# Performance work log

Hardware: AMD Instinct MI355X
Metric: run time of the kernel (lower is better)

## Reference

```python
import jax, jax.numpy as jnp
import numpy as np

N, G, C = 32, 197, 768
HEADS = 12
D = C // HEADS          # 64
HH = WW = 14            # spatial grid (L = 196)
F = WW // 2 + 1         # 8 rfft freqs
MLP = 3072
EPS = 1e-6


def _layernorm(x, w, b):
    mu = jnp.mean(x, axis=-1, keepdims=True)
    var = jnp.mean((x - mu) ** 2, axis=-1, keepdims=True)
    return (x - mu) / jnp.sqrt(var + EPS) * w + b


def setup_inputs() -> dict:
    key = jax.random.key(0)
    ks = jax.random.split(key, 16)
    std = 0.02
    return {
        "x": jax.random.normal(ks[0], (N, G, C), dtype=jnp.float32),
        "mixer": std * jax.random.normal(ks[1], (HH, F, C, C, 2), dtype=jnp.float32),
        "Q_w": std * jax.random.normal(ks[2], (D, HEADS, D), dtype=jnp.float32),
        "Q_b": std * jax.random.normal(ks[3], (1, HEADS, 1), dtype=jnp.float32),
        "K_w": std * jax.random.normal(ks[4], (D, HEADS, D), dtype=jnp.float32),
        "K_b": std * jax.random.normal(ks[5], (G, HEADS, 1), dtype=jnp.float32),
        "V_w": std * jax.random.normal(ks[6], (D, HEADS, D), dtype=jnp.float32),
        "V_b": std * jax.random.normal(ks[7], (G, HEADS, 1), dtype=jnp.float32),
        "ln2_w": jnp.ones((C,), dtype=jnp.float32),
        "ln2_b": jnp.zeros((C,), dtype=jnp.float32),
        "w1": std * jax.random.normal(ks[8], (C, MLP), dtype=jnp.float32),
        "b1": jnp.zeros((MLP,), dtype=jnp.float32),
        "w2": std * jax.random.normal(ks[9], (MLP, C), dtype=jnp.float32),
        "b2": jnp.zeros((C,), dtype=jnp.float32),
    }


def reference(x, mixer, Q_w, Q_b, K_w, K_b, V_w, V_b, ln2_w, ln2_b, w1, b1, w2, b2):
    # NOTE: original torch code computes ln_1(input) but discards it (dead code).
    cls = x[:, :1]                       # [N,1,C]
    tok = x[:, 1:]                       # [N,L,C]
    t = tok.reshape(N, HH, WW, C)
    tf = jnp.fft.rfft2(t, axes=(1, 2), norm="ortho")          # [N,H,F,C] complex64
    m = mixer[..., 0] + 1j * mixer[..., 1]                       # [H,F,C,C] complex64
    tf = jnp.einsum("nhfd,hfds->nhfd", tf, m)
    t = jnp.fft.irfft2(tf, s=(HH, WW), axes=(1, 2), norm="ortho").reshape(N, HH * WW, C)
    full = jnp.concatenate([cls, t], axis=1)                     # [N,G,C]
    Q = cls.reshape(N, 1, HEADS, D)
    K = full.reshape(N, G, HEADS, D)
    V = full.reshape(N, G, HEADS, D)
    Q = jnp.einsum("nqhd,xhd->nqhx", Q, Q_w) + Q_b
    K = jnp.einsum("nkhd,xhd->nkhx", K, K_w) + K_b
    V = jnp.einsum("nvhd,xhd->nvhx", V, V_w) + V_b
    A = jnp.einsum("nqhd,nkhd->nhqk", Q, K) / (float(D) ** 0.5)
    A = jax.nn.softmax(A, axis=3)
    new_cls = jnp.einsum("nhqk,nkhd->nqhd", A, V).reshape(N, 1, C)
    xo = jnp.concatenate([new_cls, t], axis=1) + x               # residual (dropout=identity)
    y = _layernorm(xo, ln2_w, ln2_b)
    y = jax.nn.gelu(y @ w1 + b1, approximate=False) @ w2 + b2
    return xo + y
```

## Files before the change

### kernel.cpp

```cpp
#include <hip/hip_runtime.h>
#include <hip/hip_bf16.h>

typedef unsigned short u16;
typedef short bf16x8 __attribute__((ext_vector_type(8)));
typedef float f32x4 __attribute__((ext_vector_type(4)));

#define N_ 32
#define G_ 197
#define C_ 768
#define HEADS_ 12
#define D_ 64
#define HH_ 14
#define FF_ 8
#define MLP_ 3072
#define MPAD 6400
#define MROWS 6304

__device__ __forceinline__ u16 f2bf(float f) {
    unsigned int u = __float_as_uint(f);
    u += 0x7FFF + ((u >> 16) & 1);
    return (u16)(u >> 16);
}

__global__ __launch_bounds__(256) void reduce_mixer(const float* __restrict__ mixer,
                                                    float2* __restrict__ msum) {
    int lane = threadIdx.x & 63;
    size_t widx = (size_t)blockIdx.x * 4 + (threadIdx.x >> 6);
    const float* base = mixer + widx * 1536;
    float re = 0.f, im = 0.f;
#pragma unroll
    for (int it = 0; it < 6; it++) {
        float4 v = *(const float4*)(base + it * 256 + lane * 4);
        re += v.x + v.z;
        im += v.y + v.w;
    }
#pragma unroll
    for (int o = 32; o; o >>= 1) {
        re += __shfl_xor(re, o);
        im += __shfl_xor(im, o);
    }
    if (lane == 0) msum[widx] = make_float2(re, im);
}

__global__ __launch_bounds__(256) void build_k(const float2* __restrict__ msum,
                                               float* __restrict__ kbuf) {
    int d = blockIdx.x;
    int tid = threadIdx.x;
    __shared__ float mre[112], mim[112], ct[14], st[14];
    if (tid < 112) {
        float2 v = msum[(size_t)tid * 768 + d];
        mre[tid] = v.x;
        mim[tid] = v.y;
    }
    if (tid >= 112 && tid < 126) {
        int j = tid - 112;
        float ang = 6.28318530717958647692f * (float)j / 14.f;
        ct[j] = cosf(ang);
        st[j] = sinf(ang);
    }
    __syncthreads();
    if (tid < 196) {
        int da = tid / 14, db = tid % 14;
        float acc = 0.f;
        for (int u = 0; u < 14; u++) {
            int idx = (u * da) % 14;
#pragma unroll
            for (int v = 0; v < 8; v++) {
                float w = (v == 0 || v == 7) ? 1.f : 2.f;
                acc += w * (mre[u * 8 + v] * ct[idx] - mim[u * 8 + v] * st[idx]);
                idx += db;
                if (idx >= 14) idx -= 14;
            }
        }
        kbuf[(size_t)d * 196 + tid] = acc * (1.f / 196.f);
    }
}

__device__ __forceinline__ void conv_proc(int a, int p, int lane, const float* kl,
                                          const float (&tq)[14], float (&ac)[14]) {
    int ra = a - p;
    if (ra < 0) ra += 14;
    const float* kr = &kl[lane * 197 + ra * 14];
    float kq[14];
#pragma unroll
    for (int i = 0; i < 14; i++) kq[i] = kr[i];
#pragma unroll
    for (int b = 0; b < 14; b++)
#pragma unroll
        for (int q = 0; q < 14; q++) ac[b] += tq[q] * kq[(b - q + 14) % 14];
}

__global__ __launch_bounds__(256) void conv_kernel(const float* __restrict__ x,
                                                   const float* __restrict__ kbuf,
                                                   float* __restrict__ t2) {
    __shared__ float tl[196 * 32];
    __shared__ float kl[32 * 197];
    int n = blockIdx.x / 24;
    int d0 = (blockIdx.x % 24) * 32;
    int tid = threadIdx.x;
    for (int i = tid; i < 196 * 32; i += 256) {
        int s = i >> 5, dl = i & 31;
        tl[i] = x[((size_t)n * 197 + 1 + s) * 768 + d0 + dl];
    }
    for (int i = tid; i < 32 * 196; i += 256) {
        int dl = i / 196, j = i - dl * 196;
        kl[dl * 197 + j] = kbuf[(size_t)(d0 + dl) * 196 + j];
    }
    __syncthreads();
    int lane = tid & 31, sg = tid >> 5;
    bool two = (sg < 6);
    int a0 = two ? sg * 2 : 12 + (sg - 6);
    float acc0[14], acc1[14];
#pragma unroll
    for (int i = 0; i < 14; i++) {
        acc0[i] = 0.f;
        acc1[i] = 0.f;
    }
    for (int p = 0; p < 14; p++) {
        float tq[14];
#pragma unroll
        for (int q = 0; q < 14; q++) tq[q] = tl[(p * 14 + q) * 32 + lane];
        conv_proc(a0, p, lane, kl, tq, acc0);
        if (two) conv_proc(a0 + 1, p, lane, kl, tq, acc1);
    }
    __syncthreads();
#pragma unroll
    for (int b = 0; b < 14; b++) tl[(a0 * 14 + b) * 32 + lane] = acc0[b];
    if (two) {
#pragma unroll
        for (int b = 0; b < 14; b++) tl[((a0 + 1) * 14 + b) * 32 + lane] = acc1[b];
    }
    __syncthreads();
    for (int i = tid; i < 196 * 32; i += 256) {
        int s = i >> 5, dl = i & 31;
        t2[((size_t)n * 196 + s) * 768 + d0 + dl] = tl[i];
    }
}

__device__ __forceinline__ float blk_sum(float v, float* red) {
    int lane = threadIdx.x & 63, wid = threadIdx.x >> 6;
#pragma unroll
    for (int o = 32; o; o >>= 1) v += __shfl_xor(v, o);
    if (lane == 0) red[wid] = v;
    __syncthreads();
    float r = red[0] + red[1] + red[2] + red[3];
    __syncthreads();
    return r;
}
__device__ __forceinline__ float blk_max(float v, float* red) {
    int lane = threadIdx.x & 63, wid = threadIdx.x >> 6;
#pragma unroll
    for (int o = 32; o; o >>= 1) v = fmaxf(v, __shfl_xor(v, o));
    if (lane == 0) red[wid] = v;
    __syncthreads();
    float r = fmaxf(fmaxf(red[0], red[1]), fmaxf(red[2], red[3]));
    __syncthreads();
    return r;
}

__global__ __launch_bounds__(256) void attn_kernel(
    const float* __restrict__ x, const float* __restrict__ t2, const float* __restrict__ Qw,
    const float* __restrict__ Qb, const float* __restrict__ Kw, const float* __restrict__ Kb,
    const float* __restrict__ Vw, const float* __restrict__ Vb, float* __restrict__ newcls) {
    int n = blockIdx.x / 12, h = blockIdx.x % 12;
    int tid = threadIdx.x;
    __shared__ float cls_s[64], Qp[64], gv[64], Aw[197], fv[64];
    __shared__ float red[8];
    const float* xn = x + (size_t)n * 197 * 768;
    if (tid < 64) cls_s[tid] = xn[h * 64 + tid];
    __syncthreads();
    if (tid < 64) {
        float s = 0.f;
        const float* qw = Qw + (size_t)tid * 768 + h * 64;
#pragma unroll 8
        for (int d = 0; d < 64; d++) s += cls_s[d] * qw[d];
        Qp[tid] = s + Qb[h];
    }
    __syncthreads();
    float sQ = blk_sum(tid < 64 ? Qp[tid] : 0.f, red);
    if (tid < 64) {
        float s = 0.f;
        for (int xq = 0; xq < 64; xq++) s += Qp[xq] * Kw[(size_t)xq * 768 + h * 64 + tid];
        gv[tid] = s;
    }
    __syncthreads();
    float apre = -3.0e38f;
    if (tid < 197) {
        const float* fr =
            (tid == 0) ? (xn + h * 64) : (t2 + ((size_t)n * 196 + tid - 1) * 768 + h * 64);
        float s = 0.f;
#pragma unroll 8
        for (int d = 0; d < 64; d++) s += fr[d] * gv[d];
        apre = (s + Kb[tid * 12 + h] * sQ) * 0.125f;
    }
    float mx = blk_max(apre, red);
    float p = (tid < 197) ? __expf(apre - mx) : 0.f;
    float denom = blk_sum(p, red);
    float sAV = blk_sum(tid < 197 ? p * Vb[tid * 12 + h] : 0.f, red) / denom;
    if (tid < 197) Aw[tid] = p / denom;
    __syncthreads();
    if (tid < 64) {
        float s = 0.f;
        for (int k = 0; k < 197; k++) {
            const float* fr = (k == 0) ? xn : (t2 + ((size_t)n * 196 + k - 1) * 768);
            s += Aw[k] * fr[h * 64 + tid];
        }
        fv[tid] = s;
    }
    __syncthreads();
    if (tid < 64) {
        float s = 0.f;
        for (int d = 0; d < 64; d++) s += fv[d] * Vw[(size_t)tid * 768 + h * 64 + d];
        newcls[(size_t)n * 768 + h * 64 + tid] = s + sAV;
    }
}

__global__ __launch_bounds__(256) void ln_kernel(const float* __restrict__ x,
                                                 const float* __restrict__ t2,
                                                 const float* __restrict__ newcls,
                                                 const float* __restrict__ lnw,
                                                 const float* __restrict__ lnb,
                                                 float* __restrict__ xo, u16* __restrict__ Y) {
    int row = blockIdx.x;
    int n = row / 197, g = row % 197;
    int tid = threadIdx.x;
    __shared__ float red[8], red2[8];
    const float* xr = x + (size_t)row * 768;
    const float* add = (g == 0) ? (newcls + (size_t)n * 768) : (t2 + ((size_t)n * 196 + g - 1) * 768);
    float v[3];
    float s = 0.f, s2 = 0.f;
#pragma unroll
    for (int j = 0; j < 3; j++) {
        int c = tid + j * 256;
        float t = xr[c] + add[c];
        v[j] = t;
        s += t;
        s2 += t * t;
    }
    int lane = tid & 63, wid = tid >> 6;
#pragma unroll
    for (int o = 32; o; o >>= 1) {
        s += __shfl_xor(s, o);
        s2 += __shfl_xor(s2, o);
    }
    if (lane == 0) {
        red[wid] = s;
        red2[wid] = s2;
    }
    __syncthreads();
    s = red[0] + red[1] + red[2] + red[3];
    s2 = red2[0] + red2[1] + red2[2] + red2[3];
    float mu = s * (1.f / 768.f);
    float var = s2 * (1.f / 768.f) - mu * mu;
    float rstd = 1.f / sqrtf(var + 1e-6f);
#pragma unroll
    for (int j = 0; j < 3; j++) {
        int c = tid + j * 256;
        float t = v[j];
        xo[(size_t)row * 768 + c] = t;
        float y = (t - mu) * rstd * lnw[c] + lnb[c];
        Y[(size_t)row * 768 + c] = f2bf(y);
    }
}

__global__ __launch_bounds__(256) void transpose_to_bf16(const float* __restrict__ in,
                                                         u16* __restrict__ out, int R, int C) {
    __shared__ float tile[32][33];
    int c0 = blockIdx.x * 32, r0 = blockIdx.y * 32;
    int tx = threadIdx.x & 31, ty = threadIdx.x >> 5;
    for (int j = ty; j < 32; j += 8) tile[j][tx] = in[(size_t)(r0 + j) * C + c0 + tx];
    __syncthreads();
    for (int j = ty; j < 32; j += 8) out[(size_t)(c0 + j) * R + r0 + tx] = f2bf(tile[tx][j]);
}

template <int EPI>
__global__ __launch_bounds__(256) void gemm128(const u16* __restrict__ A, const u16* __restrict__ Bt,
                                               int K, const float* __restrict__ bias,
                                               const float* __restrict__ resid,
                                               void* __restrict__ outv, int Nt) {
    __shared__ __align__(16) u16 As[128 * 32];
    __shared__ __align__(16) u16 Bs[128 * 32];
    int m0 = blockIdx.y * 128, n0 = blockIdx.x * 128;
    int tid = threadIdx.x;
    int lane = tid & 63, w = tid >> 6, wr = w >> 1, wc = w & 1;
    int lr = lane & 15, lkb = (lane >> 4) * 8;
    int arow = tid >> 2, acol = (tid & 3) * 8;

    f32x4 acc[4][4];
#pragma unroll
    for (int i = 0; i < 4; i++)
#pragma unroll
        for (int j = 0; j < 4; j++) {
            f32x4 z = {0.f, 0.f, 0.f, 0.f};
            acc[i][j] = z;
        }

    for (int k0 = 0; k0 < K; k0 += 32) {
        *(uint4*)&As[arow * 32 + acol] = *(const uint4*)&A[(size_t)(m0 + arow) * K + k0 + acol];
        *(uint4*)&As[(arow + 64) * 32 + acol] =
            *(const uint4*)&A[(size_t)(m0 + arow + 64) * K + k0 + acol];
        *(uint4*)&Bs[arow * 32 + acol] = *(const uint4*)&Bt[(size_t)(n0 + arow) * K + k0 + acol];
        *(uint4*)&Bs[(arow + 64) * 32 + acol] =
            *(const uint4*)&Bt[(size_t)(n0 + arow + 64) * K + k0 + acol];
        __syncthreads();
        bf16x8 af[4], bfr[4];
#pragma unroll
        for (int i = 0; i < 4; i++) {
            af[i] = *(const bf16x8*)&As[(wr * 64 + i * 16 + lr) * 32 + lkb];
            bfr[i] = *(const bf16x8*)&Bs[(wc * 64 + i * 16 + lr) * 32 + lkb];
        }
#pragma unroll
        for (int mi = 0; mi < 4; mi++)
#pragma unroll
            for (int ni = 0; ni < 4; ni++)
                acc[mi][ni] =
                    __builtin_amdgcn_mfma_f32_16x16x32_bf16(af[mi], bfr[ni], acc[mi][ni], 0, 0, 0);
        __syncthreads();
    }

    int rbase = (lane >> 4) * 4;
#pragma unroll
    for (int mi = 0; mi < 4; mi++)
#pragma unroll
        for (int ni = 0; ni < 4; ni++) {
            int colg = n0 + wc * 64 + ni * 16 + lr;
#pragma unroll
            for (int r = 0; r < 4; r++) {
                int rowg = m0 + wr * 64 + mi * 16 + rbase + r;
                float a = acc[mi][ni][r];
                if (EPI == 0) {
                    float h = a + bias[colg];
                    h = 0.5f * h * (1.f + erff(h * 0.70710678118654752f));
                    ((u16*)outv)[(size_t)rowg * Nt + colg] = f2bf(h);
                } else {
                    if (rowg < MROWS) {
                        float h = a + bias[colg] + resid[(size_t)rowg * 768 + colg];
                        ((float*)outv)[(size_t)rowg * Nt + colg] = h;
                    }
                }
            }
        }
}

extern "C" void kernel_launch(void* const* d_in, const int* in_sizes, int n_in, void* d_out,
                              int out_size, void* d_ws, size_t ws_size, hipStream_t stream) {
    const float* x = (const float*)d_in[0];
    const float* mixer = (const float*)d_in[1];
    const float* Qw = (const float*)d_in[2];
    const float* Qb = (const float*)d_in[3];
    const float* Kw = (const float*)d_in[4];
    const float* Kb = (const float*)d_in[5];
    const float* Vw = (const float*)d_in[6];
    const float* Vb = (const float*)d_in[7];
    const float* lnw = (const float*)d_in[8];
    const float* lnb = (const float*)d_in[9];
    const float* w1 = (const float*)d_in[10];
    const float* b1 = (const float*)d_in[11];
    const float* w2 = (const float*)d_in[12];
    const float* b2 = (const float*)d_in[13];
    char* ws = (char*)d_ws;

    size_t off = 0;
    auto alloc = [&](size_t bytes) {
        size_t o = off;
        off += (bytes + 255) & ~(size_t)255;
        return o;
    };
    float2* msum = (float2*)(ws + alloc((size_t)14 * 8 * 768 * 8));
    float* kbuf = (float*)(ws + alloc((size_t)768 * 196 * 4));
    float* t2 = (float*)(ws + alloc((size_t)32 * 196 * 768 * 4));
    float* newcls = (float*)(ws + alloc((size_t)32 * 768 * 4));
    float* xo = (float*)(ws + alloc((size_t)32 * 197 * 768 * 4));
    u16* Ybuf = (u16*)(ws + alloc((size_t)MPAD * 768 * 2));
    u16* Hbuf = (u16*)(ws + alloc((size_t)MPAD * 3072 * 2));
    u16* w1t = (u16*)(ws + alloc((size_t)3072 * 768 * 2));
    u16* w2t = (u16*)(ws + alloc((size_t)768 * 3072 * 2));
    if (off > ws_size) return;

    transpose_to_bf16<<<dim3(3072 / 32, 768 / 32), 256, 0, stream>>>(w1, w1t, 768, 3072);
    transpose_to_bf16<<<dim3(768 / 32, 3072 / 32), 256, 0, stream>>>(w2, w2t, 3072, 768);
    reduce_mixer<<<21504, 256, 0, stream>>>(mixer, msum);
    build_k<<<768, 256, 0, stream>>>(msum, kbuf);
    conv_kernel<<<768, 256, 0, stream>>>(x, kbuf, t2);
    attn_kernel<<<384, 256, 0, stream>>>(x, t2, Qw, Qb, Kw, Kb, Vw, Vb, newcls);
    ln_kernel<<<6304, 256, 0, stream>>>(x, t2, newcls, lnw, lnb, xo, Ybuf);
    gemm128<0><<<dim3(3072 / 128, 50), 256, 0, stream>>>(Ybuf, w1t, 768, b1, nullptr, Hbuf, 3072);
    gemm128<1><<<dim3(768 / 128, 50), 256, 0, stream>>>(Hbuf, w2t, 3072, b2, xo, d_out, 768);
}
```

Before: 960.1 us.

## Use direct global-to-LDS loads in MLP GEMMs and narrow second GEMM tile

Replaces the register-staged global-to-shared copies in both MLP GEMMs with the global_load_lds builtin, so each wave writes 16-byte chunks straight into LDS without passing through VGPRs. The second GEMM (N=768) now uses a 128x64 tile, doubling its block count from 300 to 600 so more CUs are busy. The narrower tile gives less reuse per block and more redundant A-tile loads. The direct-to-LDS path relies on the builtin's per-lane LDS addressing matching the row-major layout the MFMA fragment reads expect.

```diff
diff --git a/kernel.cpp b/kernel.cpp
--- a/kernel.cpp
+++ b/kernel.cpp
@@ -20,6 +20,19 @@
     unsigned int u = __float_as_uint(f);
     u += 0x7FFF + ((u >> 16) & 1);
     return (u16)(u >> 16);
+}
+
+__device__ __forceinline__ void gld16(const void* g, void* l) {
+#if __has_builtin(__builtin_amdgcn_global_load_lds)
+    auto gp = reinterpret_cast<const __attribute__((address_space(1))) unsigned int*>(
+        reinterpret_cast<uintptr_t>(g));
+    auto lp = reinterpret_cast<__attribute__((address_space(3))) unsigned int*>(
+        reinterpret_cast<uintptr_t>(l));
+    __builtin_amdgcn_global_load_lds(gp, lp, 16, 0, 0);
+#else
+    int lane = threadIdx.x & 63;
+    *(uint4*)((char*)l + lane * 16) = *(const uint4*)((const char*)g);
+#endif
 }
 
 __global__ __launch_bounds__(256) void reduce_mixer(const float* __restrict__ mixer,
@@ -273,46 +286,64 @@
     for (int j = ty; j < 32; j += 8) out[(size_t)(c0 + j) * R + r0 + tx] = f2bf(tile[tx][j]);
 }
 
-template <int EPI>
-__global__ __launch_bounds__(256) void gemm128(const u16* __restrict__ A, const u16* __restrict__ Bt,
-                                               int K, const float* __restrict__ bias,
-                                               const float* __restrict__ resid,
-                                               void* __restrict__ outv, int Nt) {
+template <int EPI, int BN>
+__global__ __launch_bounds__(256) void gemm_glds(const u16* __restrict__ A,
+                                                 const u16* __restrict__ Bt, int K,
+                                                 const float* __restrict__ bias,
+                                                 const float* __restrict__ resid,
+                                                 void* __restrict__ outv, int Nt) {
     __shared__ __align__(16) u16 As[128 * 32];
-    __shared__ __align__(16) u16 Bs[128 * 32];
-    int m0 = blockIdx.y * 128, n0 = blockIdx.x * 128;
+    __shared__ __align__(16) u16 Bs[BN * 32];
+    constexpr int NI = BN / 32;
+    int m0 = blockIdx.y * 128, n0 = blockIdx.x * BN;
     int tid = threadIdx.x;
     int lane = tid & 63, w = tid >> 6, wr = w >> 1, wc = w & 1;
     int lr = lane & 15, lkb = (lane >> 4) * 8;
-    int arow = tid >> 2, acol = (tid & 3) * 8;
-
-    f32x4 acc[4][4];
+    int lrow = lane >> 2, lcol = (lane & 3) * 8;
+
+    const u16* Ag0 = A + (size_t)(m0 + w * 32 + lrow) * K + lcol;
+    const u16* Ag1 = Ag0 + (size_t)16 * K;
+    u16* Al0 = &As[(w * 32) * 32];
+    u16* Al1 = &As[(w * 32 + 16) * 32];
+    const u16* Bg0;
+    const u16* Bg1 = nullptr;
+    u16* Bl0;
+    u16* Bl1 = nullptr;
+    if constexpr (BN == 128) {
+        Bg0 = Bt + (size_t)(n0 + w * 32 + lrow) * K + lcol;
+        Bg1 = Bg0 + (size_t)16 * K;
+        Bl0 = &Bs[(w * 32) * 32];
+        Bl1 = &Bs[(w * 32 + 16) * 32];
+    } else {
+        Bg0 = Bt + (size_t)(n0 + w * 16 + lrow) * K + lcol;
+        Bl0 = &Bs[(w * 16) * 32];
+    }
+
+    f32x4 acc[4][NI];
 #pragma unroll
     for (int i = 0; i < 4; i++)
 #pragma unroll
-        for (int j = 0; j < 4; j++) {
+        for (int j = 0; j < NI; j++) {
             f32x4 z = {0.f, 0.f, 0.f, 0.f};
             acc[i][j] = z;
         }
 
     for (int k0 = 0; k0 < K; k0 += 32) {
-        *(uint4*)&As[arow * 32 + acol] = *(const uint4*)&A[(size_t)(m0 + arow) * K + k0 + acol];
-        *(uint4*)&As[(arow + 64) * 32 + acol] =
-            *(const uint4*)&A[(size_t)(m0 + arow + 64) * K + k0 + acol];
-        *(uint4*)&Bs[arow * 32 + acol] = *(const uint4*)&Bt[(size_t)(n0 + arow) * K + k0 + acol];
-        *(uint4*)&Bs[(arow + 64) * 32 + acol] =
-            *(const uint4*)&Bt[(size_t)(n0 + arow + 64) * K + k0 + acol];
+        gld16(Ag0 + k0, Al0);
+        gld16(Ag1 + k0, Al1);
+        gld16(Bg0 + k0, Bl0);
+        if constexpr (BN == 128) gld16(Bg1 + k0, Bl1);
         __syncthreads();
-        bf16x8 af[4], bfr[4];
-#pragma unroll
-        for (int i = 0; i < 4; i++) {
-            af[i] = *(const bf16x8*)&As[(wr * 64 + i * 16 + lr) * 32 + lkb];
-            bfr[i] = *(const bf16x8*)&Bs[(wc * 64 + i * 16 + lr) * 32 + lkb];
-        }
+        bf16x8 af[4], bfr[NI];
+#pragma unroll
+        for (int i = 0; i < 4; i++) af[i] = *(const bf16x8*)&As[(wr * 64 + i * 16 + lr) * 32 + lkb];
+#pragma unroll
+        for (int i = 0; i < NI; i++)
+            bfr[i] = *(const bf16x8*)&Bs[(wc * (BN / 2) + i * 16 + lr) * 32 + lkb];
 #pragma unroll
         for (int mi = 0; mi < 4; mi++)
 #pragma unroll
-            for (int ni = 0; ni < 4; ni++)
+            for (int ni = 0; ni < NI; ni++)
                 acc[mi][ni] =
                     __builtin_amdgcn_mfma_f32_16x16x32_bf16(af[mi], bfr[ni], acc[mi][ni], 0, 0, 0);
         __syncthreads();
@@ -322,8 +353,8 @@
 #pragma unroll
     for (int mi = 0; mi < 4; mi++)
 #pragma unroll
-        for (int ni = 0; ni < 4; ni++) {
-            int colg = n0 + wc * 64 + ni * 16 + lr;
+        for (int ni = 0; ni < NI; ni++) {
+            int colg = n0 + wc * (BN / 2) + ni * 16 + lr;
 #pragma unroll
             for (int r = 0; r < 4; r++) {
                 int rowg = m0 + wr * 64 + mi * 16 + rbase + r;
@@ -384,6 +415,6 @@
     conv_kernel<<<768, 256, 0, stream>>>(x, kbuf, t2);
     attn_kernel<<<384, 256, 0, stream>>>(x, t2, Qw, Qb, Kw, Kb, Vw, Vb, newcls);
     ln_kernel<<<6304, 256, 0, stream>>>(x, t2, newcls, lnw, lnb, xo, Ybuf);
-    gemm128<0><<<dim3(3072 / 128, 50), 256, 0, stream>>>(Ybuf, w1t, 768, b1, nullptr, Hbuf, 3072);
-    gemm128<1><<<dim3(768 / 128, 50), 256, 0, stream>>>(Hbuf, w2t, 3072, b2, xo, d_out, 768);
-}
+    gemm_glds<0, 128><<<dim3(3072 / 128, 50), 256, 0, stream>>>(Ybuf, w1t, 768, b1, nullptr, Hbuf, 3072);
+    gemm_glds<1, 64><<<dim3(768 / 64, 50), 256, 0, stream>>>(Hbuf, w2t, 3072, b2, xo, d_out, 768);
+}
```

Measured after the change: 939.3 us. 2.2% less time.

## Use direct global-to-LDS loads in GEMMs and split-K the second MLP GEMM

Applied to the files above, without the earlier changes.

The GEMM tile loads now go through global_load_lds, which writes straight into shared memory and skips the register round-trip. The second GEMM (K=3072, only 300 blocks) is split into two K halves over gridDim.z so more blocks run on the device. The fp32 partial results go to a workspace and are summed with bias and residual in a new combine kernel. The two weight-transpose launches are also merged into one. The cost is extra partial-buffer traffic and one more launch, and the LDS-direct layout relies on each wave writing 64 contiguous 16-byte chunks.

```diff
diff --git a/kernel.cpp b/kernel.cpp
--- a/kernel.cpp
+++ b/kernel.cpp
@@ -20,6 +20,19 @@
     unsigned int u = __float_as_uint(f);
     u += 0x7FFF + ((u >> 16) & 1);
     return (u16)(u >> 16);
+}
+
+__device__ __forceinline__ void gld16(const void* g, void* l) {
+#if __has_builtin(__builtin_amdgcn_global_load_lds)
+    auto gp = reinterpret_cast<const __attribute__((address_space(1))) unsigned int*>(
+        reinterpret_cast<uintptr_t>(g));
+    auto lp = reinterpret_cast<__attribute__((address_space(3))) unsigned int*>(
+        reinterpret_cast<uintptr_t>(l));
+    __builtin_amdgcn_global_load_lds(gp, lp, 16, 0, 0);
+#else
+    int lane = threadIdx.x & 63;
+    *(uint4*)((char*)l + lane * 16) = *(const uint4*)((const char*)g);
+#endif
 }
 
 __global__ __launch_bounds__(256) void reduce_mixer(const float* __restrict__ mixer,
@@ -263,10 +276,23 @@
     }
 }
 
-__global__ __launch_bounds__(256) void transpose_to_bf16(const float* __restrict__ in,
-                                                         u16* __restrict__ out, int R, int C) {
+__global__ __launch_bounds__(256) void transpose_both(const float* __restrict__ w1,
+                                                      const float* __restrict__ w2,
+                                                      u16* __restrict__ w1t,
+                                                      u16* __restrict__ w2t) {
     __shared__ float tile[32][33];
-    int c0 = blockIdx.x * 32, r0 = blockIdx.y * 32;
+    int bid = blockIdx.x;
+    const float* in;
+    u16* out;
+    int R, C, c0, r0;
+    if (bid < 2304) {
+        in = w1; out = w1t; R = 768; C = 3072;
+        c0 = (bid % 96) * 32; r0 = (bid / 96) * 32;
+    } else {
+        int b2 = bid - 2304;
+        in = w2; out = w2t; R = 3072; C = 768;
+        c0 = (b2 % 24) * 32; r0 = (b2 / 24) * 32;
+    }
     int tx = threadIdx.x & 31, ty = threadIdx.x >> 5;
     for (int j = ty; j < 32; j += 8) tile[j][tx] = in[(size_t)(r0 + j) * C + c0 + tx];
     __syncthreads();
@@ -274,17 +300,28 @@
 }
 
 template <int EPI>
-__global__ __launch_bounds__(256) void gemm128(const u16* __restrict__ A, const u16* __restrict__ Bt,
-                                               int K, const float* __restrict__ bias,
-                                               const float* __restrict__ resid,
-                                               void* __restrict__ outv, int Nt) {
+__global__ __launch_bounds__(256) void gemm_glds(const u16* __restrict__ A,
+                                                 const u16* __restrict__ Bt, int K,
+                                                 const float* __restrict__ bias,
+                                                 void* __restrict__ outv, int Nt) {
     __shared__ __align__(16) u16 As[128 * 32];
     __shared__ __align__(16) u16 Bs[128 * 32];
     int m0 = blockIdx.y * 128, n0 = blockIdx.x * 128;
     int tid = threadIdx.x;
     int lane = tid & 63, w = tid >> 6, wr = w >> 1, wc = w & 1;
     int lr = lane & 15, lkb = (lane >> 4) * 8;
-    int arow = tid >> 2, acol = (tid & 3) * 8;
+    int lrow = lane >> 2, lcol = (lane & 3) * 8;
+    int kspan = K / gridDim.z;
+    int kbeg = blockIdx.z * kspan, kend = kbeg + kspan;
+
+    const u16* Ag0 = A + (size_t)(m0 + w * 32 + lrow) * K + lcol;
+    const u16* Ag1 = Ag0 + (size_t)16 * K;
+    u16* Al0 = &As[(w * 32) * 32];
+    u16* Al1 = &As[(w * 32 + 16) * 32];
+    const u16* Bg0 = Bt + (size_t)(n0 + w * 32 + lrow) * K + lcol;
+    const u16* Bg1 = Bg0 + (size_t)16 * K;
+    u16* Bl0 = &Bs[(w * 32) * 32];
+    u16* Bl1 = &Bs[(w * 32 + 16) * 32];
 
     f32x4 acc[4][4];
 #pragma unroll
@@ -295,13 +332,11 @@
             acc[i][j] = z;
         }
 
-    for (int k0 = 0; k0 < K; k0 += 32) {
-        *(uint4*)&As[arow * 32 + acol] = *(const uint4*)&A[(size_t)(m0 + arow) * K + k0 + acol];
-        *(uint4*)&As[(arow + 64) * 32 + acol] =
-            *(const uint4*)&A[(size_t)(m0 + arow + 64) * K + k0 + acol];
-        *(uint4*)&Bs[arow * 32 + acol] = *(const uint4*)&Bt[(size_t)(n0 + arow) * K + k0 + acol];
-        *(uint4*)&Bs[(arow + 64) * 32 + acol] =
-            *(const uint4*)&Bt[(size_t)(n0 + arow + 64) * K + k0 + acol];
+    for (int k0 = kbeg; k0 < kend; k0 += 32) {
+        gld16(Ag0 + k0, Al0);
+        gld16(Ag1 + k0, Al1);
+        gld16(Bg0 + k0, Bl0);
+        gld16(Bg1 + k0, Bl1);
         __syncthreads();
         bf16x8 af[4], bfr[4];
 #pragma unroll
@@ -319,6 +354,7 @@
     }
 
     int rbase = (lane >> 4) * 4;
+    float* pout = (float*)outv + (size_t)blockIdx.z * MPAD * Nt;
 #pragma unroll
     for (int mi = 0; mi < 4; mi++)
 #pragma unroll
@@ -333,13 +369,29 @@
                     h = 0.5f * h * (1.f + erff(h * 0.70710678118654752f));
                     ((u16*)outv)[(size_t)rowg * Nt + colg] = f2bf(h);
                 } else {
-                    if (rowg < MROWS) {
-                        float h = a + bias[colg] + resid[(size_t)rowg * 768 + colg];
-                        ((float*)outv)[(size_t)rowg * Nt + colg] = h;
-                    }
+                    pout[(size_t)rowg * Nt + colg] = a;
                 }
             }
         }
+}
+
+__global__ __launch_bounds__(256) void combine_out(const float* __restrict__ part,
+                                                   const float* __restrict__ b2,
+                                                   const float* __restrict__ xo,
+                                                   float* __restrict__ out) {
+    int idx = blockIdx.x * 256 + threadIdx.x;
+    if (idx >= MROWS * 768 / 4) return;
+    int c = (idx * 4) % 768;
+    const float4 p0 = *(const float4*)&part[(size_t)idx * 4];
+    const float4 p1 = *(const float4*)&part[(size_t)MPAD * 768 + idx * 4];
+    const float4 rz = *(const float4*)&xo[(size_t)idx * 4];
+    const float4 bb = *(const float4*)&b2[c];
+    float4 o;
+    o.x = p0.x + p1.x + rz.x + bb.x;
+    o.y = p0.y + p1.y + rz.y + bb.y;
+    o.z = p0.z + p1.z + rz.z + bb.z;
+    o.w = p0.w + p1.w + rz.w + bb.w;
+    *(float4*)&out[(size_t)idx * 4] = o;
 }
 
 extern "C" void kernel_launch(void* const* d_in, const int* in_sizes, int n_in, void* d_out,
@@ -375,15 +427,16 @@
     u16* Hbuf = (u16*)(ws + alloc((size_t)MPAD * 3072 * 2));
     u16* w1t = (u16*)(ws + alloc((size_t)3072 * 768 * 2));
     u16* w2t = (u16*)(ws + alloc((size_t)768 * 3072 * 2));
+    float* part = (float*)(ws + alloc((size_t)2 * MPAD * 768 * 4));
     if (off > ws_size) return;
 
-    transpose_to_bf16<<<dim3(3072 / 32, 768 / 32), 256, 0, stream>>>(w1, w1t, 768, 3072);
-    transpose_to_bf16<<<dim3(768 / 32, 3072 / 32), 256, 0, stream>>>(w2, w2t, 3072, 768);
+    transpose_both<<<4608, 256, 0, stream>>>(w1, w2, w1t, w2t);
     reduce_mixer<<<21504, 256, 0, stream>>>(mixer, msum);
     build_k<<<768, 256, 0, stream>>>(msum, kbuf);
     conv_kernel<<<768, 256, 0, stream>>>(x, kbuf, t2);
     attn_kernel<<<384, 256, 0, stream>>>(x, t2, Qw, Qb, Kw, Kb, Vw, Vb, newcls);
     ln_kernel<<<6304, 256, 0, stream>>>(x, t2, newcls, lnw, lnb, xo, Ybuf);
-    gemm128<0><<<dim3(3072 / 128, 50), 256, 0, stream>>>(Ybuf, w1t, 768, b1, nullptr, Hbuf, 3072);
-    gemm128<1><<<dim3(768 / 128, 50), 256, 0, stream>>>(Hbuf, w2t, 3072, b2, xo, d_out, 768);
-}
+    gemm_glds<0><<<dim3(3072 / 128, 50, 1), 256, 0, stream>>>(Ybuf, w1t, 768, b1, Hbuf, 3072);
+    gemm_glds<2><<<dim3(768 / 128, 50, 2), 256, 0, stream>>>(Hbuf, w2t, 3072, nullptr, part, 768);
+    combine_out<<<(MROWS * 768 / 4 + 255) / 256, 256, 0, stream>>>(part, b2, xo, (float*)d_out);
+}
```

Measured after the change: 935.9 us. 1.03x faster.
